# Optimization experiments

Measured on AMD Instinct MI355X. Metric: run time of the kernel, lower is better.

The kernel has to match this reference:

```python
import jax, jax.numpy as jnp
import numpy as np

TOP_K = 2
NUM_EXPERTS = 8


def setup_inputs() -> dict:
    key = jax.random.key(0)
    ks = jax.random.split(key, 9)
    B, S, N, H = 1, 8, 1024, 512
    E, I_moe, I_sh = NUM_EXPERTS, 2048 // TOP_K, 2048
    s = 0.02
    return {
        "hidden_states": jax.random.normal(ks[0], (B, S, N, H), dtype=jnp.float32),
        "gate_w": jax.random.normal(ks[1], (E, H), dtype=jnp.float32) * s,
        "expert_w1": jax.random.normal(ks[2], (E, I_moe, H), dtype=jnp.float32) * s,
        "expert_w2": jax.random.normal(ks[3], (E, H, I_moe), dtype=jnp.float32) * s,
        "expert_w3": jax.random.normal(ks[4], (E, I_moe, H), dtype=jnp.float32) * s,
        "shared_w1": jax.random.normal(ks[5], (I_sh, H), dtype=jnp.float32) * s,
        "shared_w2": jax.random.normal(ks[6], (H, I_sh), dtype=jnp.float32) * s,
        "shared_w3": jax.random.normal(ks[7], (I_sh, H), dtype=jnp.float32) * s,
        "shared_gate_w": jax.random.normal(ks[8], (1, H), dtype=jnp.float32) * s,
    }


def reference(hidden_states, gate_w, expert_w1, expert_w2, expert_w3,
              shared_w1, shared_w2, shared_w3, shared_gate_w):
    B, S, N, H = hidden_states.shape
    x = hidden_states.reshape(-1, H)                       # [T, H], T = B*S*N

    # Router: softmax in fp32, then top-k (norm_topk_prob=False).
    router_logits = x @ gate_w.T                           # [T, E]
    probs = jax.nn.softmax(router_logits.astype(jnp.float32), axis=-1)
    top_w, top_i = jax.lax.top_k(probs, TOP_K)             # [T, k]
    # Combine weight per (token, expert): zero for unselected experts.
    combine = jnp.sum(top_w[..., None] * jax.nn.one_hot(top_i, NUM_EXPERTS, dtype=probs.dtype), axis=1)
    combine = combine.astype(x.dtype)                      # [T, E]

    # Routed experts (SwiGLU FFN per expert), evaluated densely and masked
    # by the sparse combine weights (same math as gather/scatter dispatch).
    h1 = jnp.einsum('th,eih->tei', x, expert_w1)           # [T, E, I_moe]
    h3 = jnp.einsum('th,eih->tei', x, expert_w3)
    h = jax.nn.silu(h1) * h3
    expert_out = jnp.einsum('tei,ehi->teh', h, expert_w2)  # [T, E, H]
    moe_out = jnp.einsum('te,teh->th', combine, expert_out)

    # Shared expert with sigmoid gate.
    sh = (jax.nn.silu(x @ shared_w1.T) * (x @ shared_w3.T)) @ shared_w2.T
    sgate = jax.nn.sigmoid(x @ shared_gate_w.T)            # [T, 1]
    out = moe_out + sgate * sh

    return out.reshape(B, S, N, H), router_logits
```

## Files before the change

kernel.cpp:

```cpp
#include <hip/hip_runtime.h>
#include <hip/hip_bf16.h>
#include <stdint.h>
#include <math.h>

typedef __bf16 bf16;
typedef bf16 bf16x8 __attribute__((ext_vector_type(8)));
typedef bf16 bf16x4 __attribute__((ext_vector_type(4)));
typedef float f32x4 __attribute__((ext_vector_type(4)));
typedef unsigned int u32;

#define TOKENS 8192
#define HD 512
#define NE 8
#define IM 1024
#define ISH 2048
#define CAP 2560

__device__ __forceinline__ void gld16(const void* g, void* l) {
  __builtin_amdgcn_global_load_lds(
      (const __attribute__((address_space(1))) u32*)g,
      (__attribute__((address_space(3))) u32*)l, 16, 0, 0);
}

#define F4_X  (TOKENS * HD / 4)
#define F4_E  (NE * IM * HD / 4)
#define F4_S  (ISH * HD / 4)
#define F4_B1 (F4_X)
#define F4_B2 (F4_B1 + F4_E)
#define F4_B3 (F4_B2 + F4_E)
#define F4_B4 (F4_B3 + F4_S)
#define F4_B5 (F4_B4 + F4_S)
#define F4_B6 (F4_B5 + F4_E)
#define F4_TOT (F4_B6 + F4_S)

__global__ void cvt_all(const float* __restrict__ x, const float* __restrict__ e1,
                        const float* __restrict__ e3, const float* __restrict__ s1,
                        const float* __restrict__ s3, const float* __restrict__ e2,
                        const float* __restrict__ s2, bf16* __restrict__ dst) {
  int i = blockIdx.x * 256 + threadIdx.x;
  if (i >= F4_TOT) return;
  const float* s; int off;
  if (i < F4_B1)      { s = x;  off = i; }
  else if (i < F4_B2) { s = e1; off = i - F4_B1; }
  else if (i < F4_B3) { s = e3; off = i - F4_B2; }
  else if (i < F4_B4) { s = s1; off = i - F4_B3; }
  else if (i < F4_B5) { s = s3; off = i - F4_B4; }
  else if (i < F4_B6) { s = e2; off = i - F4_B5; }
  else                { s = s2; off = i - F4_B6; }
  const float4 v = ((const float4*)s)[off];
  bf16x4 o;
  o.x = (bf16)v.x; o.y = (bf16)v.y; o.z = (bf16)v.z; o.w = (bf16)v.w;
  ((bf16x4*)dst)[i] = o;
}

__launch_bounds__(256)
__global__ void router_k(const float* __restrict__ x, const float* __restrict__ gw,
                         const float* __restrict__ sgw, float* __restrict__ logits,
                         float* __restrict__ sgate, int* __restrict__ topi,
                         float* __restrict__ topw, int* __restrict__ counts) {
  if (blockIdx.x == 0 && threadIdx.x < NE) counts[threadIdx.x] = 0;
  __shared__ float gws[9][512];
  for (int i = threadIdx.x; i < 9 * 512; i += 256) {
    int r = i >> 9, c = i & 511;
    gws[r][c] = (r < 8) ? gw[i] : sgw[c];
  }
  __syncthreads();
  int wave = threadIdx.x >> 6, lane = threadIdx.x & 63;
  int t = blockIdx.x * 4 + wave;
  const float* xp = x + (size_t)t * HD;
  float xv[8];
#pragma unroll
  for (int j = 0; j < 8; j++) xv[j] = xp[lane + 64 * j];
  float acc[9];
#pragma unroll
  for (int e = 0; e < 9; e++) {
    float a = 0.f;
#pragma unroll
    for (int j = 0; j < 8; j++) a = fmaf(xv[j], gws[e][lane + 64 * j], a);
    acc[e] = a;
  }
#pragma unroll
  for (int off = 32; off > 0; off >>= 1) {
#pragma unroll
    for (int e = 0; e < 9; e++) acc[e] += __shfl_down(acc[e], off);
  }
  if (lane == 0) {
    float mx = acc[0];
#pragma unroll
    for (int e = 1; e < 8; e++) mx = fmaxf(mx, acc[e]);
    float p[8], sum = 0.f;
#pragma unroll
    for (int e = 0; e < 8; e++) { p[e] = expf(acc[e] - mx); sum += p[e]; }
    float inv = 1.f / sum;
    int i0 = 0; float b0 = p[0];
#pragma unroll
    for (int e = 1; e < 8; e++) if (p[e] > b0) { b0 = p[e]; i0 = e; }
    int i1 = -1; float b1 = -1.f;
#pragma unroll
    for (int e = 0; e < 8; e++) if (e != i0 && p[e] > b1) { b1 = p[e]; i1 = e; }
#pragma unroll
    for (int e = 0; e < 8; e++) logits[(size_t)t * 8 + e] = acc[e];
    topi[2 * t] = i0; topi[2 * t + 1] = i1;
    topw[2 * t] = b0 * inv; topw[2 * t + 1] = b1 * inv;
    sgate[t] = 1.f / (1.f + expf(-acc[8]));
  }
}

__launch_bounds__(256)
__global__ void dispatch_k(const int* __restrict__ topi, const float* __restrict__ topw,
                           int* __restrict__ counts, int* __restrict__ tok,
                           float* __restrict__ wl, int* __restrict__ pos) {
  __shared__ int lcnt[NE];
  __shared__ int lbase[NE];
  int tid = threadIdx.x;
  if (tid < NE) lcnt[tid] = 0;
  __syncthreads();
  int t = blockIdx.x * 256 + tid;
  int e0 = topi[2 * t], e1 = topi[2 * t + 1];
  float w0 = topw[2 * t], w1 = topw[2 * t + 1];
  int r0 = atomicAdd(&lcnt[e0], 1);
  int r1 = atomicAdd(&lcnt[e1], 1);
  __syncthreads();
  if (tid < NE) lbase[tid] = atomicAdd(&counts[tid], lcnt[tid]);
  __syncthreads();
  int p0 = lbase[e0] + r0;
  int p1 = lbase[e1] + r1;
  if (p0 < CAP) { tok[e0 * CAP + p0] = t; wl[e0 * CAP + p0] = w0; }
  if (p1 < CAP) { tok[e1 * CAP + p1] = t; wl[e1 * CAP + p1] = w1; }
  pos[2 * t]     = (p0 < CAP) ? e0 * CAP + p0 : -1;
  pos[2 * t + 1] = (p1 < CAP) ? e1 * CAP + p1 : -1;
}

__launch_bounds__(256, 2)
__global__ void gemm1_k(const bf16* __restrict__ X, const int* __restrict__ tokl,
                        const int* __restrict__ counts,
                        const bf16* __restrict__ e1w, const bf16* __restrict__ e3w,
                        const bf16* __restrict__ s1w, const bf16* __restrict__ s3w,
                        bf16* __restrict__ hmoe, bf16* __restrict__ hsh) {
  const bf16 *W1, *W3;
  bf16* Hout;
  const int* tl = nullptr;
  int cnt = 0, m0, n0, N;
  bool gather;
  int y = blockIdx.y;
  if (y < 160) {
    int e = y / 20, mt = y % 20;
    cnt = min(counts[e], CAP);
    if (mt * 128 >= cnt) return;
    gather = true;
    tl = tokl + e * CAP;
    W1 = e1w + (size_t)e * IM * HD;
    W3 = e3w + (size_t)e * IM * HD;
    Hout = hmoe + (size_t)e * CAP * IM;
    N = IM; m0 = mt * 128; n0 = blockIdx.x * 64;
  } else {
    int s = y - 160;
    gather = false;
    W1 = s1w; W3 = s3w; Hout = hsh; N = ISH;
    m0 = (s >> 1) * 128;
    n0 = ((s & 1) * 16 + blockIdx.x) * 64;
  }

  __shared__ __align__(16) bf16 As[2][128 * 32];
  __shared__ __align__(16) bf16 B1s[2][64 * 32];
  __shared__ __align__(16) bf16 B3s[2][64 * 32];

  int tid = threadIdx.x;
  int sr = tid >> 2;
  int colb = (tid & 3) * 16;
  int ar0, ar1;
  if (gather) {
    ar0 = tl[min(m0 + sr, cnt - 1)];
    ar1 = tl[min(m0 + 64 + sr, cnt - 1)];
  } else { ar0 = m0 + sr; ar1 = m0 + 64 + sr; }
  const char* apa = (const char*)(X + (size_t)ar0 * HD) + colb;
  const char* apb = (const char*)(X + (size_t)ar1 * HD) + colb;
  const char* bp1 = (const char*)(W1 + (size_t)(n0 + sr) * HD) + colb;
  const char* bp3 = (const char*)(W3 + (size_t)(n0 + sr) * HD) + colb;
  char* lA0a = (char*)&As[0][0] + tid * 16;
  char* lA0b = (char*)&As[1][0] + tid * 16;
  char* lA1a = (char*)&As[0][0] + 4096 + tid * 16;
  char* lA1b = (char*)&As[1][0] + 4096 + tid * 16;
  char* lB1a = (char*)&B1s[0][0] + tid * 16;
  char* lB1b = (char*)&B1s[1][0] + tid * 16;
  char* lB3a = (char*)&B3s[0][0] + tid * 16;
  char* lB3b = (char*)&B3s[1][0] + tid * 16;

  int wid = tid >> 6, lane = tid & 63;
  int wm = (wid >> 1) * 64, wn = (wid & 1) * 32;
  int lrow = lane & 15, lq = lane >> 4;

  f32x4 acc1[4][2] = {};
  f32x4 acc3[4][2] = {};

  for (int kb = 0; kb < 1024; kb += 128) {
    __syncthreads();
    gld16(apa + kb, lA0a);      gld16(apa + kb + 64, lA0b);
    gld16(apb + kb, lA1a);      gld16(apb + kb + 64, lA1b);
    gld16(bp1 + kb, lB1a);      gld16(bp1 + kb + 64, lB1b);
    gld16(bp3 + kb, lB3a);      gld16(bp3 + kb + 64, lB3b);
    __syncthreads();
#pragma unroll
    for (int ks = 0; ks < 2; ks++) {
      bf16x8 a[4], b1[2], b3[2];
#pragma unroll
      for (int i = 0; i < 4; i++)
        a[i] = *(const bf16x8*)&As[ks][(wm + i * 16 + lrow) * 32 + lq * 8];
#pragma unroll
      for (int j = 0; j < 2; j++) {
        b1[j] = *(const bf16x8*)&B1s[ks][(wn + j * 16 + lrow) * 32 + lq * 8];
        b3[j] = *(const bf16x8*)&B3s[ks][(wn + j * 16 + lrow) * 32 + lq * 8];
      }
#pragma unroll
      for (int i = 0; i < 4; i++)
#pragma unroll
        for (int j = 0; j < 2; j++) {
          acc1[i][j] = __builtin_amdgcn_mfma_f32_16x16x32_bf16(a[i], b1[j], acc1[i][j], 0, 0, 0);
          acc3[i][j] = __builtin_amdgcn_mfma_f32_16x16x32_bf16(a[i], b3[j], acc3[i][j], 0, 0, 0);
        }
    }
  }

#pragma unroll
  for (int i = 0; i < 4; i++)
#pragma unroll
    for (int r = 0; r < 4; r++) {
      int row = m0 + wm + i * 16 + lq * 4 + r;
#pragma unroll
      for (int j = 0; j < 2; j++) {
        float v1 = acc1[i][j][r], v3 = acc3[i][j][r];
        float hv = v1 / (1.f + __expf(-v1)) * v3;
        Hout[(size_t)row * N + (n0 + wn + j * 16 + lrow)] = (bf16)hv;
      }
    }
}

__launch_bounds__(256, 2)
__global__ void gemm2_k(const bf16* __restrict__ hmoe, const bf16* __restrict__ hsh,
                        const bf16* __restrict__ e2w, const bf16* __restrict__ s2w,
                        const float* __restrict__ wll, const int* __restrict__ counts,
                        bf16* __restrict__ yslot, bf16* __restrict__ ysh) {
  const bf16 *Hin, *W2;
  const float* wlp = nullptr;
  bf16* Yout;
  int cnt = 0, m0, K;
  bool weighted;
  int y = blockIdx.y;
  if (y < 160) {
    int e = y / 20, mt = y % 20;
    cnt = min(counts[e], CAP);
    if (mt * 128 >= cnt) return;
    weighted = true;
    Hin = hmoe + (size_t)e * CAP * IM;
    W2 = e2w + (size_t)e * HD * IM;
    wlp = wll + e * CAP;
    Yout = yslot + (size_t)e * CAP * HD;
    K = IM; m0 = mt * 128;
  } else {
    weighted = false;
    Hin = hsh; W2 = s2w; Yout = ysh; K = ISH; m0 = (y - 160) * 128;
  }
  int n0 = blockIdx.x * 128;

  __shared__ __align__(16) bf16 As[128 * 32];
  __shared__ __align__(16) bf16 Bs[128 * 32];

  int tid = threadIdx.x;
  int sr = tid >> 2;
  int colb = (tid & 3) * 16;
  const char* apa = (const char*)(Hin + (size_t)(m0 + sr) * K) + colb;
  const char* apb = (const char*)(Hin + (size_t)(m0 + 64 + sr) * K) + colb;
  const char* bpa = (const char*)(W2 + (size_t)(n0 + sr) * K) + colb;
  const char* bpb = (const char*)(W2 + (size_t)(n0 + 64 + sr) * K) + colb;
  char* lA0 = (char*)As + tid * 16;
  char* lA1 = (char*)As + 4096 + tid * 16;
  char* lB0 = (char*)Bs + tid * 16;
  char* lB1 = (char*)Bs + 4096 + tid * 16;

  int wid = tid >> 6, lane = tid & 63;
  int wm = (wid >> 1) * 64, wn = (wid & 1) * 64;
  int lrow = lane & 15, lq = lane >> 4;

  f32x4 acc[4][4] = {};

  for (int kb = 0; kb < K * 2; kb += 64) {
    __syncthreads();
    gld16(apa + kb, lA0);
    gld16(apb + kb, lA1);
    gld16(bpa + kb, lB0);
    gld16(bpb + kb, lB1);
    __syncthreads();
    bf16x8 a[4], b[4];
#pragma unroll
    for (int i = 0; i < 4; i++) {
      a[i] = *(const bf16x8*)&As[(wm + i * 16 + lrow) * 32 + lq * 8];
      b[i] = *(const bf16x8*)&Bs[(wn + i * 16 + lrow) * 32 + lq * 8];
    }
#pragma unroll
    for (int i = 0; i < 4; i++)
#pragma unroll
      for (int j = 0; j < 4; j++)
        acc[i][j] = __builtin_amdgcn_mfma_f32_16x16x32_bf16(a[i], b[j], acc[i][j], 0, 0, 0);
  }

#pragma unroll
  for (int i = 0; i < 4; i++)
#pragma unroll
    for (int r = 0; r < 4; r++) {
      int row = m0 + wm + i * 16 + lq * 4 + r;
      float w = weighted ? ((row < cnt) ? wlp[row] : 0.f) : 1.f;
      bf16* op = Yout + (size_t)row * HD;
#pragma unroll
      for (int j = 0; j < 4; j++)
        op[n0 + wn + j * 16 + lrow] = (bf16)(w * acc[i][j][r]);
    }
}

__launch_bounds__(256)
__global__ void combine_k(const bf16* __restrict__ yslot, const bf16* __restrict__ ysh,
                          const int* __restrict__ pos, const float* __restrict__ sgate,
                          float* __restrict__ out) {
  int wave = threadIdx.x >> 6, lane = threadIdx.x & 63;
  int t = blockIdx.x * 4 + wave;
  int p0 = pos[2 * t], p1 = pos[2 * t + 1];
  float g = sgate[t];
  int col = lane * 8;
  float acc[8];
  {
    const bf16x8 s = *(const bf16x8*)(ysh + (size_t)t * HD + col);
#pragma unroll
    for (int i = 0; i < 8; i++) acc[i] = g * (float)s[i];
  }
  if (p0 >= 0) {
    const bf16x8 v = *(const bf16x8*)(yslot + (size_t)p0 * HD + col);
#pragma unroll
    for (int i = 0; i < 8; i++) acc[i] += (float)v[i];
  }
  if (p1 >= 0) {
    const bf16x8 v = *(const bf16x8*)(yslot + (size_t)p1 * HD + col);
#pragma unroll
    for (int i = 0; i < 8; i++) acc[i] += (float)v[i];
  }
  float* op = out + (size_t)t * HD + col;
#pragma unroll
  for (int i = 0; i < 8; i++) op[i] = acc[i];
}

extern "C" void kernel_launch(void* const* d_in, const int* in_sizes, int n_in,
                              void* d_out, int out_size, void* d_ws, size_t ws_size,
                              hipStream_t stream) {
  const float* x   = (const float*)d_in[0];
  const float* gw  = (const float*)d_in[1];
  const float* ew1 = (const float*)d_in[2];
  const float* ew2 = (const float*)d_in[3];
  const float* ew3 = (const float*)d_in[4];
  const float* sw1 = (const float*)d_in[5];
  const float* sw2 = (const float*)d_in[6];
  const float* sw3 = (const float*)d_in[7];
  const float* sgw = (const float*)d_in[8];
  float* out = (float*)d_out;
  float* logits = out + (size_t)TOKENS * HD;

  char* w = (char*)d_ws;
  bf16* xb  = (bf16*)w; w += (size_t)TOKENS * HD * 2;
  bf16* e1b = (bf16*)w; w += (size_t)NE * IM * HD * 2;
  bf16* e3b = (bf16*)w; w += (size_t)NE * IM * HD * 2;
  bf16* s1b = (bf16*)w; w += (size_t)ISH * HD * 2;
  bf16* s3b = (bf16*)w; w += (size_t)ISH * HD * 2;
  bf16* e2b = (bf16*)w; w += (size_t)NE * HD * IM * 2;
  bf16* s2b = (bf16*)w; w += (size_t)HD * ISH * 2;
  float* sgate = (float*)w; w += TOKENS * 4;
  int*   topi  = (int*)w;   w += TOKENS * 2 * 4;
  float* topw  = (float*)w; w += TOKENS * 2 * 4;
  int*   counts = (int*)w;  w += 256;
  int*   tok   = (int*)w;   w += NE * CAP * 4;
  float* wl    = (float*)w; w += NE * CAP * 4;
  int*   pos   = (int*)w;   w += TOKENS * 2 * 4;
  bf16* hmoe = (bf16*)w; w += (size_t)NE * CAP * IM * 2;
  bf16* hsh  = (bf16*)w; w += (size_t)TOKENS * ISH * 2;
  bf16* yslot = xb;
  bf16* ysh   = (bf16*)((char*)xb + (size_t)NE * CAP * HD * 2);

  hipLaunchKernelGGL(cvt_all, dim3((F4_TOT + 255) / 256), dim3(256), 0, stream,
                     x, ew1, ew3, sw1, sw3, ew2, sw2, xb);
  hipLaunchKernelGGL(router_k, dim3(TOKENS / 4), dim3(256), 0, stream,
                     x, gw, sgw, logits, sgate, topi, topw, counts);
  hipLaunchKernelGGL(dispatch_k, dim3(TOKENS / 256), dim3(256), 0, stream,
                     topi, topw, counts, tok, wl, pos);
  hipLaunchKernelGGL(gemm1_k, dim3(16, 160 + 128), dim3(256), 0, stream,
                     xb, tok, counts, e1b, e3b, s1b, s3b, hmoe, hsh);
  hipLaunchKernelGGL(gemm2_k, dim3(4, 160 + 64), dim3(256), 0, stream,
                     hmoe, hsh, e2b, s2b, wl, counts, yslot, ysh);
  hipLaunchKernelGGL(combine_k, dim3(TOKENS / 4), dim3(256), 0, stream,
                     yslot, ysh, pos, sgate, out);
}
```

Baseline: 295.4 us.

## Fuse x bf16 conversion into router, raise occupancy bounds, reorder gemm2 blocks

The fp32-to-bf16 conversion of the activations moves from the bulk conversion kernel into the router kernel. The router already reads each token row, so the activations are read once instead of twice, and the router load becomes contiguous float4 loads with a transposed LDS layout for the gate weights. Launch bounds for both GEMMs go from 2 to 4 waves-per-EU minimum, which may force register spilling. gemm2 now schedules the shared-expert tiles before the routed-expert tiles so the long K=2048 blocks start first.

```diff
diff --git a/kernel.cpp b/kernel.cpp
--- a/kernel.cpp
+++ b/kernel.cpp
@@ -22,31 +22,28 @@
       (__attribute__((address_space(3))) u32*)l, 16, 0, 0);
 }
 
-#define F4_X  (TOKENS * HD / 4)
 #define F4_E  (NE * IM * HD / 4)
 #define F4_S  (ISH * HD / 4)
-#define F4_B1 (F4_X)
-#define F4_B2 (F4_B1 + F4_E)
-#define F4_B3 (F4_B2 + F4_E)
-#define F4_B4 (F4_B3 + F4_S)
-#define F4_B5 (F4_B4 + F4_S)
-#define F4_B6 (F4_B5 + F4_E)
-#define F4_TOT (F4_B6 + F4_S)
-
-__global__ void cvt_all(const float* __restrict__ x, const float* __restrict__ e1,
-                        const float* __restrict__ e3, const float* __restrict__ s1,
-                        const float* __restrict__ s3, const float* __restrict__ e2,
-                        const float* __restrict__ s2, bf16* __restrict__ dst) {
+#define F4_C1 (F4_E)
+#define F4_C2 (F4_C1 + F4_E)
+#define F4_C3 (F4_C2 + F4_S)
+#define F4_C4 (F4_C3 + F4_S)
+#define F4_C5 (F4_C4 + F4_E)
+#define F4_TOT (F4_C5 + F4_S)
+
+__global__ void cvt_all(const float* __restrict__ e1, const float* __restrict__ e3,
+                        const float* __restrict__ s1, const float* __restrict__ s3,
+                        const float* __restrict__ e2, const float* __restrict__ s2,
+                        bf16* __restrict__ dst) {
   int i = blockIdx.x * 256 + threadIdx.x;
   if (i >= F4_TOT) return;
   const float* s; int off;
-  if (i < F4_B1)      { s = x;  off = i; }
-  else if (i < F4_B2) { s = e1; off = i - F4_B1; }
-  else if (i < F4_B3) { s = e3; off = i - F4_B2; }
-  else if (i < F4_B4) { s = s1; off = i - F4_B3; }
-  else if (i < F4_B5) { s = s3; off = i - F4_B4; }
-  else if (i < F4_B6) { s = e2; off = i - F4_B5; }
-  else                { s = s2; off = i - F4_B6; }
+  if (i < F4_C1)      { s = e1; off = i; }
+  else if (i < F4_C2) { s = e3; off = i - F4_C1; }
+  else if (i < F4_C3) { s = s1; off = i - F4_C2; }
+  else if (i < F4_C4) { s = s3; off = i - F4_C3; }
+  else if (i < F4_C5) { s = e2; off = i - F4_C4; }
+  else                { s = s2; off = i - F4_C5; }
   const float4 v = ((const float4*)s)[off];
   bf16x4 o;
   o.x = (bf16)v.x; o.y = (bf16)v.y; o.z = (bf16)v.z; o.w = (bf16)v.w;
@@ -57,26 +54,34 @@
 __global__ void router_k(const float* __restrict__ x, const float* __restrict__ gw,
                          const float* __restrict__ sgw, float* __restrict__ logits,
                          float* __restrict__ sgate, int* __restrict__ topi,
-                         float* __restrict__ topw, int* __restrict__ counts) {
+                         float* __restrict__ topw, int* __restrict__ counts,
+                         bf16* __restrict__ xb) {
   if (blockIdx.x == 0 && threadIdx.x < NE) counts[threadIdx.x] = 0;
   __shared__ float gws[9][512];
   for (int i = threadIdx.x; i < 9 * 512; i += 256) {
     int r = i >> 9, c = i & 511;
-    gws[r][c] = (r < 8) ? gw[i] : sgw[c];
+    float v = (r < 8) ? gw[i] : sgw[c];
+    gws[r][((c & 7) << 6) | (c >> 3)] = v;
   }
   __syncthreads();
   int wave = threadIdx.x >> 6, lane = threadIdx.x & 63;
   int t = blockIdx.x * 4 + wave;
-  const float* xp = x + (size_t)t * HD;
-  float xv[8];
-#pragma unroll
-  for (int j = 0; j < 8; j++) xv[j] = xp[lane + 64 * j];
+  const float* xp = x + (size_t)t * HD + lane * 8;
+  float4 va = *(const float4*)xp;
+  float4 vb = *(const float4*)(xp + 4);
+  float xv[8] = {va.x, va.y, va.z, va.w, vb.x, vb.y, vb.z, vb.w};
+  {
+    bf16x8 xo;
+#pragma unroll
+    for (int j = 0; j < 8; j++) xo[j] = (bf16)xv[j];
+    *(bf16x8*)(xb + (size_t)t * HD + lane * 8) = xo;
+  }
   float acc[9];
 #pragma unroll
   for (int e = 0; e < 9; e++) {
     float a = 0.f;
 #pragma unroll
-    for (int j = 0; j < 8; j++) a = fmaf(xv[j], gws[e][lane + 64 * j], a);
+    for (int j = 0; j < 8; j++) a = fmaf(xv[j], gws[e][j * 64 + lane], a);
     acc[e] = a;
   }
 #pragma unroll
@@ -131,7 +136,7 @@
   pos[2 * t + 1] = (p1 < CAP) ? e1 * CAP + p1 : -1;
 }
 
-__launch_bounds__(256, 2)
+__launch_bounds__(256, 4)
 __global__ void gemm1_k(const bf16* __restrict__ X, const int* __restrict__ tokl,
                         const int* __restrict__ counts,
                         const bf16* __restrict__ e1w, const bf16* __restrict__ e3w,
@@ -235,7 +240,7 @@
     }
 }
 
-__launch_bounds__(256, 2)
+__launch_bounds__(256, 4)
 __global__ void gemm2_k(const bf16* __restrict__ hmoe, const bf16* __restrict__ hsh,
                         const bf16* __restrict__ e2w, const bf16* __restrict__ s2w,
                         const float* __restrict__ wll, const int* __restrict__ counts,
@@ -246,8 +251,11 @@
   int cnt = 0, m0, K;
   bool weighted;
   int y = blockIdx.y;
-  if (y < 160) {
-    int e = y / 20, mt = y % 20;
+  if (y < 64) {
+    weighted = false;
+    Hin = hsh; W2 = s2w; Yout = ysh; K = ISH; m0 = y * 128;
+  } else {
+    int e = (y - 64) / 20, mt = (y - 64) % 20;
     cnt = min(counts[e], CAP);
     if (mt * 128 >= cnt) return;
     weighted = true;
@@ -256,9 +264,6 @@
     wlp = wll + e * CAP;
     Yout = yslot + (size_t)e * CAP * HD;
     K = IM; m0 = mt * 128;
-  } else {
-    weighted = false;
-    Hin = hsh; W2 = s2w; Yout = ysh; K = ISH; m0 = (y - 160) * 128;
   }
   int n0 = blockIdx.x * 128;
 
@@ -382,14 +387,14 @@
   bf16* ysh   = (bf16*)((char*)xb + (size_t)NE * CAP * HD * 2);
 
   hipLaunchKernelGGL(cvt_all, dim3((F4_TOT + 255) / 256), dim3(256), 0, stream,
-                     x, ew1, ew3, sw1, sw3, ew2, sw2, xb);
+                     ew1, ew3, sw1, sw3, ew2, sw2, e1b);
   hipLaunchKernelGGL(router_k, dim3(TOKENS / 4), dim3(256), 0, stream,
-                     x, gw, sgw, logits, sgate, topi, topw, counts);
+                     x, gw, sgw, logits, sgate, topi, topw, counts, xb);
   hipLaunchKernelGGL(dispatch_k, dim3(TOKENS / 256), dim3(256), 0, stream,
                      topi, topw, counts, tok, wl, pos);
   hipLaunchKernelGGL(gemm1_k, dim3(16, 160 + 128), dim3(256), 0, stream,
                      xb, tok, counts, e1b, e3b, s1b, s3b, hmoe, hsh);
-  hipLaunchKernelGGL(gemm2_k, dim3(4, 160 + 64), dim3(256), 0, stream,
+  hipLaunchKernelGGL(gemm2_k, dim3(4, 64 + 160), dim3(256), 0, stream,
                      hmoe, hsh, e2b, s2b, wl, counts, yslot, ysh);
   hipLaunchKernelGGL(combine_k, dim3(TOKENS / 4), dim3(256), 0, stream,
                      yslot, ysh, pos, sgate, out);
```

After: 286.3 us. 1.03x faster.
